# Kernel optimization log

Hardware: AMD Instinct MI355X
Metric: run time of the kernel (lower is better)

The kernel has to match this reference:

```python
import jax, jax.numpy as jnp
import numpy as np

B, N, DIM = 4, 4096, 512
H, DH = 8, 64
F = 256          # nb_features = min(256, int(log(4096)*32)) = 256
CS = 128         # chunk_size = min(128, n)


def setup_inputs() -> dict:
    key = jax.random.key(0)
    k1, k2, k3, k4 = jax.random.split(key, 4)
    x = jax.random.normal(k1, (B, N, DIM), jnp.float32)
    # scale linear weights like default init so activations stay well-conditioned
    w_qkv = jax.random.normal(k2, (3 * H * DH, DIM), jnp.float32) / jnp.sqrt(DIM)
    w_out = jax.random.normal(k3, (DIM, H * DH), jnp.float32) / jnp.sqrt(H * DH)
    b_out = jnp.zeros((DIM,), jnp.float32)
    # torch.qr(randn(F, DH)) -> reduced Q of shape (F, DH), orthonormal columns
    proj = jnp.linalg.qr(jax.random.normal(k4, (F, DH), jnp.float32))[0]
    return {"x": x, "w_qkv": w_qkv, "w_out": w_out, "b_out": b_out, "proj": proj}


def _kernel_fn(t, proj):
    # exp(x @ proj^T - rowmax), stabilized over the feature axis (as in source)
    tp = jnp.einsum('...d,fd->...f', t, proj)
    return jnp.exp(tp - jnp.max(tp, axis=-1, keepdims=True))


def reference(x, w_qkv, w_out, b_out, proj):
    b, n, _ = x.shape
    scale = DH ** -0.5
    c = n // CS  # number of independent local chunks

    qkv = x @ w_qkv.T                                   # [b, n, 3*h*d]
    q, k, v = jnp.split(qkv, 3, axis=-1)

    def to_chunks(t):  # [b, n, h*d] -> [b, h, c, cs, d]
        return t.reshape(b, n, H, DH).transpose(0, 2, 1, 3).reshape(b, H, c, CS, DH)

    q = to_chunks(q) * scale
    k = to_chunks(k)
    v = to_chunks(v)

    q_prime = _kernel_fn(q, proj)                       # [b, h, c, cs, f]
    k_prime = _kernel_fn(k, proj)                       # [b, h, c, cs, f]

    k_sum = k_prime.sum(axis=3)                         # [b, h, c, f]
    D = jnp.einsum('bhcsf,bhcf->bhcs', q_prime, k_sum)
    D_inv = 1.0 / (D + 0.0001)

    context = jnp.einsum('bhcsf,bhcsd->bhcfd', k_prime, v)     # [b, h, c, f, d]
    out = jnp.einsum('bhcsf,bhcfd->bhcsd', q_prime, context)   # [b, h, c, cs, d]
    out = out * D_inv[..., None]

    out = out.reshape(b, H, n, DH).transpose(0, 2, 1, 3).reshape(b, n, H * DH)
    return out @ w_out.T + b_out                        # dropout p=0 -> identity
```

## Files before the change

### kernel.cpp

```cpp
#include <hip/hip_runtime.h>

#define B_ 4
#define N_ 4096
#define DIM_ 512
#define H_ 8
#define DH_ 64
#define F_ 256
#define CS_ 128
#define M_ (B_*N_)
#define NCHUNK_ 1024

typedef __attribute__((ext_vector_type(8))) short bf16x8;
typedef __attribute__((ext_vector_type(4))) float f32x4;

__device__ __forceinline__ unsigned short f2bf(float x){
  unsigned int u = __float_as_uint(x);
  u += 0x7fffu + ((u >> 16) & 1u);
  return (unsigned short)(u >> 16);
}
__device__ __forceinline__ float bf2f(unsigned short s){
  return __uint_as_float(((unsigned int)s) << 16);
}
__device__ __forceinline__ unsigned pack2(float a, float b){
  return (unsigned)f2bf(a) | ((unsigned)f2bf(b) << 16);
}
__device__ __forceinline__ void gl2lds16(const unsigned short* g, unsigned short* l) {
  __builtin_amdgcn_global_load_lds((const __attribute__((address_space(1))) unsigned int*)g,
                                   (__attribute__((address_space(3))) unsigned int*)l,
                                   16, 0, 0);
}

__global__ __launch_bounds__(256)
void split_kernel(const float* __restrict__ src, unsigned short* __restrict__ hi,
                  unsigned short* __restrict__ lo, int n4)
{
  int idx = blockIdx.x * 256 + threadIdx.x;
  if (idx >= n4) return;
  float4 v = ((const float4*)src)[idx];
  unsigned short h0 = f2bf(v.x), h1 = f2bf(v.y), h2 = f2bf(v.z), h3 = f2bf(v.w);
  unsigned short e0 = f2bf(v.x - bf2f(h0)), e1 = f2bf(v.y - bf2f(h1));
  unsigned short e2 = f2bf(v.z - bf2f(h2)), e3 = f2bf(v.w - bf2f(h3));
  uint2 hv, lv;
  hv.x = (unsigned)h0 | ((unsigned)h1 << 16); hv.y = (unsigned)h2 | ((unsigned)h3 << 16);
  lv.x = (unsigned)e0 | ((unsigned)e1 << 16); lv.y = (unsigned)e2 | ((unsigned)e3 << 16);
  ((uint2*)hi)[idx] = hv;
  ((uint2*)lo)[idx] = lv;
}

__global__ __launch_bounds__(256)
void prep_proj(const float* __restrict__ proj, unsigned short* __restrict__ pq,
               unsigned short* __restrict__ pk)
{
  int idx = blockIdx.x * 256 + threadIdx.x;
  if (idx >= 4096) return;
  float4 v = ((const float4*)proj)[idx];
  uint2 k, q;
  k.x = pack2(v.x, v.y);           k.y = pack2(v.z, v.w);
  q.x = pack2(v.x*0.125f, v.y*0.125f); q.y = pack2(v.z*0.125f, v.w*0.125f);
  ((uint2*)pk)[idx] = k;
  ((uint2*)pq)[idx] = q;
}

template<int SPLIT, int OUT>
__global__ __launch_bounds__(256, 2)
void mfma_gemm_nt(const unsigned short* __restrict__ Ahi, const unsigned short* __restrict__ Alo,
                  const unsigned short* __restrict__ Bhi, const unsigned short* __restrict__ Blo,
                  void* __restrict__ Cm, const float* __restrict__ bias, int K, int ldc,
                  unsigned short* __restrict__ vth, unsigned short* __restrict__ vtl)
{
  __shared__ __align__(16) unsigned short sAhi[4096];
  __shared__ __align__(16) unsigned short sBhi[4096];
  __shared__ __align__(16) unsigned short sAlo[4096];
  __shared__ __align__(16) unsigned short sBlo[4096];
  const int tid = threadIdx.x, lane = tid & 63, wave = tid >> 6;
  const int bm = blockIdx.y * 128, bn = blockIdx.x * 128;
  const int srow0 = wave * 32 + (lane >> 2);
  const int srow1 = srow0 + 16;
  const int slot = lane & 3;
  const int g0 = slot ^ ((srow0 >> 1) & 3);
  const int g1 = slot ^ ((srow1 >> 1) & 3);
  const size_t aOff0 = (size_t)(bm + srow0) * K + g0 * 8;
  const size_t aOff1 = (size_t)(bm + srow1) * K + g1 * 8;
  const size_t bOff0 = (size_t)(bn + srow0) * K + g0 * 8;
  const size_t bOff1 = (size_t)(bn + srow1) * K + g1 * 8;
  const int l0 = wave * 1024, l1 = wave * 1024 + 512;
  const int fr = lane & 15, quad = lane >> 4;
  const int wr = (wave >> 1) * 64, wc = (wave & 1) * 64;
  int offA[4], offB[4];
#pragma unroll
  for (int i = 0; i < 4; ++i) {
    int ra = wr + i * 16 + fr;  offA[i] = ra * 32 + (quad ^ ((ra >> 1) & 3)) * 8;
    int rb = wc + i * 16 + fr;  offB[i] = rb * 32 + (quad ^ ((rb >> 1) & 3)) * 8;
  }
  f32x4 acc[4][4];
#pragma unroll
  for (int i = 0; i < 4; ++i)
#pragma unroll
    for (int j = 0; j < 4; ++j) acc[i][j] = {0.f, 0.f, 0.f, 0.f};

  for (int k0 = 0; k0 < K; k0 += 32) {
    gl2lds16(Ahi + aOff0 + k0, &sAhi[l0]);
    gl2lds16(Ahi + aOff1 + k0, &sAhi[l1]);
    gl2lds16(Bhi + bOff0 + k0, &sBhi[l0]);
    gl2lds16(Bhi + bOff1 + k0, &sBhi[l1]);
    if (SPLIT) {
      gl2lds16(Alo + aOff0 + k0, &sAlo[l0]);
      gl2lds16(Alo + aOff1 + k0, &sAlo[l1]);
      gl2lds16(Blo + bOff0 + k0, &sBlo[l0]);
      gl2lds16(Blo + bOff1 + k0, &sBlo[l1]);
    }
    __syncthreads();
    bf16x8 ah[4], bh[4], al[4], bl[4];
#pragma unroll
    for (int i = 0; i < 4; ++i) {
      ah[i] = *(const bf16x8*)&sAhi[offA[i]];
      bh[i] = *(const bf16x8*)&sBhi[offB[i]];
      if (SPLIT) {
        al[i] = *(const bf16x8*)&sAlo[offA[i]];
        bl[i] = *(const bf16x8*)&sBlo[offB[i]];
      }
    }
#pragma unroll
    for (int i = 0; i < 4; ++i)
#pragma unroll
      for (int j = 0; j < 4; ++j) {
        acc[i][j] = __builtin_amdgcn_mfma_f32_16x16x32_bf16(ah[i], bh[j], acc[i][j], 0, 0, 0);
        if (SPLIT) {
          acc[i][j] = __builtin_amdgcn_mfma_f32_16x16x32_bf16(ah[i], bl[j], acc[i][j], 0, 0, 0);
          acc[i][j] = __builtin_amdgcn_mfma_f32_16x16x32_bf16(al[i], bh[j], acc[i][j], 0, 0, 0);
        }
      }
    __syncthreads();
  }
#pragma unroll
  for (int j = 0; j < 4; ++j) {
    int col = bn + wc + j * 16 + fr;
    float bv = (OUT == 0 && bias) ? bias[col] : 0.f;
#pragma unroll
    for (int i = 0; i < 4; ++i) {
      int row0 = bm + wr + i * 16 + quad * 4;
      if (OUT == 0) {
        float* cp = (float*)Cm + (size_t)row0 * ldc + col;
#pragma unroll
        for (int r = 0; r < 4; ++r) cp[(size_t)r * ldc] = acc[i][j][r] + bv;
      } else if (OUT == 1) {
        unsigned short* cp = (unsigned short*)Cm + (size_t)row0 * ldc + col;
#pragma unroll
        for (int r = 0; r < 4; ++r) cp[(size_t)r * ldc] = f2bf(acc[i][j][r]);
      } else {
        int hh = col >> 6, d = col & 63;
        int bb = row0 >> 12, cc2 = (row0 >> 7) & 31, s = row0 & 127;
        int ck = bb * 256 + hh * 32 + cc2;
        size_t ad = (size_t)ck * 8192 + d * 128 + (((s >> 3) ^ (d & 15)) << 3) + (s & 7);
        float v0 = acc[i][j][0], v1 = acc[i][j][1], v2 = acc[i][j][2], v3 = acc[i][j][3];
        unsigned short h0 = f2bf(v0), h1 = f2bf(v1), h2 = f2bf(v2), h3 = f2bf(v3);
        uint2 hv, lv;
        hv.x = (unsigned)h0 | ((unsigned)h1 << 16);
        hv.y = (unsigned)h2 | ((unsigned)h3 << 16);
        lv.x = pack2(v0 - bf2f(h0), v1 - bf2f(h1));
        lv.y = pack2(v2 - bf2f(h2), v3 - bf2f(h3));
        *(uint2*)(vth + ad) = hv;
        *(uint2*)(vtl + ad) = lv;
      }
    }
  }
}

__global__ __launch_bounds__(256, 1)
void fused_chunk(const unsigned short* __restrict__ qkv_bf,
                 const unsigned short* __restrict__ projq,
                 const unsigned short* __restrict__ projk,
                 const unsigned short* __restrict__ vth_g,
                 const unsigned short* __restrict__ vtl_g,
                 unsigned short* __restrict__ attn_hi,
                 unsigned short* __restrict__ attn_lo)
{
  __shared__ __align__(16) char smem[153088];
  unsigned short* KPT = (unsigned short*)smem;
  unsigned short* QP  = (unsigned short*)(smem + 65536);
  unsigned short* X   = (unsigned short*)(smem + 131072);
  float* KS  = (float*)(smem + 147456);
  float* DI  = (float*)(smem + 148480);
  float* KSP = (float*)(smem + 148992);

  const int tid = threadIdx.x, lane = tid & 63, wave = tid >> 6;
  const int fr = lane & 15, quad = lane >> 4;
  const int chunk = blockIdx.x;
  const int b = chunk >> 8, h = (chunk >> 5) & 7, cc = chunk & 31;
  const int mbase = b * N_ + cc * CS_;

#pragma unroll
  for (int j = 0; j < 8; ++j) {
    int idx = tid + j * 256;
    int s = idx >> 4, d0 = (idx & 15) * 4;
    uint2 v = *(const uint2*)(qkv_bf + (size_t)(mbase + s) * 1024 + 512 + h * DH_ + d0);
    *(uint2*)(X + s * 64 + (((d0 >> 3) ^ (s & 7)) << 3) + (d0 & 7)) = v;
  }
  __syncthreads();

  {
    f32x4 ka[2][16];
#pragma unroll
    for (int nt = 0; nt < 16; ++nt) { ka[0][nt] = {0,0,0,0}; ka[1][nt] = {0,0,0,0}; }
#pragma unroll
    for (int ks = 0; ks < 2; ++ks) {
      bf16x8 a[2];
#pragma unroll
      for (int mt = 0; mt < 2; ++mt) {
        int s = wave * 32 + mt * 16 + fr;
        a[mt] = *(const bf16x8*)(X + s * 64 + (((ks * 4 + quad) ^ (s & 7)) << 3));
      }
#pragma unroll
      for (int nt = 0; nt < 16; ++nt) {
        bf16x8 bf = *(const bf16x8*)(projk + (size_t)(nt * 16 + fr) * 64 + ks * 32 + quad * 8);
        ka[0][nt] = __builtin_amdgcn_mfma_f32_16x16x32_bf16(a[0], bf, ka[0][nt], 0, 0, 0);
        ka[1][nt] = __builtin_amdgcn_mfma_f32_16x16x32_bf16(a[1], bf, ka[1][nt], 0, 0, 0);
      }
    }
#pragma unroll
    for (int mt = 0; mt < 2; ++mt)
#pragma unroll
      for (int r = 0; r < 4; ++r) {
        float m = ka[mt][0][r];
#pragma unroll
        for (int nt = 1; nt < 16; ++nt) m = fmaxf(m, ka[mt][nt][r]);
        m = fmaxf(m, __shfl_xor(m, 1, 16));
        m = fmaxf(m, __shfl_xor(m, 2, 16));
        m = fmaxf(m, __shfl_xor(m, 4, 16));
        m = fmaxf(m, __shfl_xor(m, 8, 16));
#pragma unroll
        for (int nt = 0; nt < 16; ++nt) ka[mt][nt][r] = __expf(ka[mt][nt][r] - m);
      }
#pragma unroll
    for (int nt = 0; nt < 16; ++nt) {
      float sm = 0.f;
#pragma unroll
      for (int mt = 0; mt < 2; ++mt)
#pragma unroll
        for (int r = 0; r < 4; ++r) sm += ka[mt][nt][r];
      sm += __shfl_xor(sm, 16, 64);
      sm += __shfl_xor(sm, 32, 64);
      if (quad == 0) KSP[wave * 256 + nt * 16 + fr] = sm;
    }
#pragma unroll
    for (int nt = 0; nt < 16; ++nt) {
      int f = nt * 16 + fr;
#pragma unroll
      for (int mt = 0; mt < 2; ++mt) {
        int g = wave * 4 + mt * 2 + (quad >> 1);
        uint2 w;
        w.x = pack2(ka[mt][nt][0], ka[mt][nt][1]);
        w.y = pack2(ka[mt][nt][2], ka[mt][nt][3]);
        *(uint2*)(KPT + f * 128 + ((g ^ (f & 15)) << 3) + (quad & 1) * 4) = w;
      }
    }
  }
  __syncthreads();

  KS[tid] = KSP[tid] + KSP[256 + tid] + KSP[512 + tid] + KSP[768 + tid];
#pragma unroll
  for (int j = 0; j < 8; ++j) {
    int idx = tid + j * 256;
    int s = idx >> 4, d0 = (idx & 15) * 4;
    uint2 v = *(const uint2*)(qkv_bf + (size_t)(mbase + s) * 1024 + h * DH_ + d0);
    *(uint2*)(X + s * 64 + (((d0 >> 3) ^ (s & 7)) << 3) + (d0 & 7)) = v;
  }
  __syncthreads();

  {
    f32x4 qa[16][2];
#pragma unroll
    for (int mt = 0; mt < 16; ++mt) { qa[mt][0] = {0,0,0,0}; qa[mt][1] = {0,0,0,0}; }
#pragma unroll
    for (int ks = 0; ks < 2; ++ks) {
      bf16x8 bfr[2];
#pragma unroll
      for (int nt = 0; nt < 2; ++nt) {
        int s = wave * 32 + nt * 16 + fr;
        bfr[nt] = *(const bf16x8*)(X + s * 64 + (((ks * 4 + quad) ^ (s & 7)) << 3));
      }
#pragma unroll
      for (int mt = 0; mt < 16; ++mt) {
        bf16x8 af = *(const bf16x8*)(projq + (size_t)(mt * 16 + fr) * 64 + ks * 32 + quad * 8);
        qa[mt][0] = __builtin_amdgcn_mfma_f32_16x16x32_bf16(af, bfr[0], qa[mt][0], 0, 0, 0);
        qa[mt][1] = __builtin_amdgcn_mfma_f32_16x16x32_bf16(af, bfr[1], qa[mt][1], 0, 0, 0);
      }
    }
#pragma unroll
    for (int nt = 0; nt < 2; ++nt) {
      float m = -1e30f;
#pragma unroll
      for (int mt = 0; mt < 16; ++mt)
#pragma unroll
        for (int r = 0; r < 4; ++r) m = fmaxf(m, qa[mt][nt][r]);
      m = fmaxf(m, __shfl_xor(m, 16, 64));
      m = fmaxf(m, __shfl_xor(m, 32, 64));
#pragma unroll
      for (int mt = 0; mt < 16; ++mt)
#pragma unroll
        for (int r = 0; r < 4; ++r) qa[mt][nt][r] = __expf(qa[mt][nt][r] - m);
    }
#pragma unroll
    for (int nt = 0; nt < 2; ++nt) {
      int s = wave * 32 + nt * 16 + fr;
#pragma unroll
      for (int mt = 0; mt < 16; ++mt) {
        int g = mt * 2 + (quad >> 1);
        uint2 w;
        w.x = pack2(qa[mt][nt][0], qa[mt][nt][1]);
        w.y = pack2(qa[mt][nt][2], qa[mt][nt][3]);
        *(uint2*)(QP + s * 256 + ((g ^ (s & 15)) << 3) + (quad & 1) * 4) = w;
      }
    }
  }
  __syncthreads();

  const unsigned short* vhs = vth_g + (size_t)chunk * 8192;
  const unsigned short* vls = vtl_g + (size_t)chunk * 8192;
#pragma unroll
  for (int i = 0; i < 4; ++i) gl2lds16(vhs + (wave*4+i)*512 + lane*8, X + (wave*4+i)*512);
  __syncthreads();

  f32x4 acc_a[4][4];
#pragma unroll
  for (int i = 0; i < 4; ++i)
#pragma unroll
    for (int j = 0; j < 4; ++j) acc_a[i][j] = {0.f, 0.f, 0.f, 0.f};
#pragma unroll
  for (int ks = 0; ks < 4; ++ks) {
    int l = ks * 4 + quad;
    bf16x8 a[4];
#pragma unroll
    for (int mt = 0; mt < 4; ++mt) {
      int f = wave * 64 + mt * 16 + fr;
      a[mt] = *(const bf16x8*)(KPT + f * 128 + ((l ^ (f & 15)) << 3));
    }
#pragma unroll
    for (int nt = 0; nt < 4; ++nt) {
      int d = nt * 16 + fr;
      bf16x8 bh = *(const bf16x8*)(X + d * 128 + ((l ^ (d & 15)) << 3));
#pragma unroll
      for (int mt = 0; mt < 4; ++mt)
        acc_a[mt][nt] = __builtin_amdgcn_mfma_f32_16x16x32_bf16(a[mt], bh, acc_a[mt][nt], 0, 0, 0);
    }
  }
  __syncthreads();
#pragma unroll
  for (int i = 0; i < 4; ++i) gl2lds16(vls + (wave*4+i)*512 + lane*8, X + (wave*4+i)*512);
  __syncthreads();
#pragma unroll
  for (int ks = 0; ks < 4; ++ks) {
    int l = ks * 4 + quad;
    bf16x8 a[4];
#pragma unroll
    for (int mt = 0; mt < 4; ++mt) {
      int f = wave * 64 + mt * 16 + fr;
      a[mt] = *(const bf16x8*)(KPT + f * 128 + ((l ^ (f & 15)) << 3));
    }
#pragma unroll
    for (int nt = 0; nt < 4; ++nt) {
      int d = nt * 16 + fr;
      bf16x8 bl = *(const bf16x8*)(X + d * 128 + ((l ^ (d & 15)) << 3));
#pragma unroll
      for (int mt = 0; mt < 4; ++mt)
        acc_a[mt][nt] = __builtin_amdgcn_mfma_f32_16x16x32_bf16(a[mt], bl, acc_a[mt][nt], 0, 0, 0);
    }
  }
  __syncthreads();

#pragma unroll
  for (int mt = 0; mt < 4; ++mt)
#pragma unroll
    for (int nt = 0; nt < 4; ++nt) {
      int f0 = wave * 64 + mt * 16 + quad * 4;
      int d = nt * 16 + fr;
      int g = wave * 8 + mt * 2 + (quad >> 1);
      float v0 = acc_a[mt][nt][0], v1 = acc_a[mt][nt][1];
      float v2 = acc_a[mt][nt][2], v3 = acc_a[mt][nt][3];
      unsigned short h0 = f2bf(v0), h1 = f2bf(v1), h2 = f2bf(v2), h3 = f2bf(v3);
      uint2 whi, wlo;
      whi.x = (unsigned)h0 | ((unsigned)h1 << 16);
      whi.y = (unsigned)h2 | ((unsigned)h3 << 16);
      wlo.x = pack2(v0 - bf2f(h0), v1 - bf2f(h1));
      wlo.y = pack2(v2 - bf2f(h2), v3 - bf2f(h3));
      int ad = d * 256 + ((g ^ (d & 15)) << 3) + (quad & 1) * 4;
      *(uint2*)(KPT + ad) = whi;
      *(uint2*)(KPT + 16384 + ad) = wlo;
      (void)f0;
    }
  __syncthreads();

  if (tid < 128) {
    int s = tid;
    float dp = 0.f;
#pragma unroll 4
    for (int l = 0; l < 32; ++l) {
      bf16x8 qv = *(const bf16x8*)(QP + s * 256 + ((l ^ (s & 15)) << 3));
      f32x4 k0 = *(const f32x4*)(KS + l * 8);
      f32x4 k1 = *(const f32x4*)(KS + l * 8 + 4);
      dp += bf2f((unsigned short)qv[0]) * k0[0];
      dp += bf2f((unsigned short)qv[1]) * k0[1];
      dp += bf2f((unsigned short)qv[2]) * k0[2];
      dp += bf2f((unsigned short)qv[3]) * k0[3];
      dp += bf2f((unsigned short)qv[4]) * k1[0];
      dp += bf2f((unsigned short)qv[5]) * k1[1];
      dp += bf2f((unsigned short)qv[6]) * k1[2];
      dp += bf2f((unsigned short)qv[7]) * k1[3];
    }
    DI[s] = 1.f / (dp + 1e-4f);
  }
  __syncthreads();

  f32x4 acc2[4][2];
#pragma unroll
  for (int i = 0; i < 4; ++i) { acc2[i][0] = {0,0,0,0}; acc2[i][1] = {0,0,0,0}; }
#pragma unroll
  for (int ks = 0; ks < 8; ++ks) {
    int l = ks * 4 + quad;
    bf16x8 ah[4], al[4];
#pragma unroll
    for (int mt = 0; mt < 4; ++mt) {
      int d = mt * 16 + fr;
      int ad = d * 256 + ((l ^ (d & 15)) << 3);
      ah[mt] = *(const bf16x8*)(KPT + ad);
      al[mt] = *(const bf16x8*)(KPT + 16384 + ad);
    }
#pragma unroll
    for (int nt = 0; nt < 2; ++nt) {
      int s = wave * 32 + nt * 16 + fr;
      bf16x8 bq = *(const bf16x8*)(QP + s * 256 + ((l ^ (s & 15)) << 3));
#pragma unroll
      for (int mt = 0; mt < 4; ++mt) {
        acc2[mt][nt] = __builtin_amdgcn_mfma_f32_16x16x32_bf16(ah[mt], bq, acc2[mt][nt], 0, 0, 0);
        acc2[mt][nt] = __builtin_amdgcn_mfma_f32_16x16x32_bf16(al[mt], bq, acc2[mt][nt], 0, 0, 0);
      }
    }
  }
#pragma unroll
  for (int nt = 0; nt < 2; ++nt) {
    int s = wave * 32 + nt * 16 + fr;
    float di = DI[s];
    size_t base = (size_t)(mbase + s) * 512 + h * DH_;
#pragma unroll
    for (int mt = 0; mt < 4; ++mt) {
      int d0 = mt * 16 + quad * 4;
      float o0 = acc2[mt][nt][0] * di, o1 = acc2[mt][nt][1] * di;
      float o2 = acc2[mt][nt][2] * di, o3 = acc2[mt][nt][3] * di;
      unsigned short h0 = f2bf(o0), h1 = f2bf(o1), h2 = f2bf(o2), h3 = f2bf(o3);
      uint2 whi, wlo;
      whi.x = (unsigned)h0 | ((unsigned)h1 << 16);
      whi.y = (unsigned)h2 | ((unsigned)h3 << 16);
      wlo.x = pack2(o0 - bf2f(h0), o1 - bf2f(h1));
      wlo.y = pack2(o2 - bf2f(h2), o3 - bf2f(h3));
      *(uint2*)(attn_hi + base + d0) = whi;
      *(uint2*)(attn_lo + base + d0) = wlo;
    }
  }
}

extern "C" void kernel_launch(void* const* d_in, const int* in_sizes, int n_in,
                              void* d_out, int out_size, void* d_ws, size_t ws_size,
                              hipStream_t stream)
{
  const float* x     = (const float*)d_in[0];
  const float* w_qkv = (const float*)d_in[1];
  const float* w_out = (const float*)d_in[2];
  const float* b_out = (const float*)d_in[3];
  const float* proj  = (const float*)d_in[4];
  float* out = (float*)d_out;

  char* ws = (char*)d_ws;
  unsigned short* qkv_bf = (unsigned short*)ws;
  unsigned short* x_hi   = (unsigned short*)(ws + 33554432);
  unsigned short* x_lo   = x_hi + (size_t)M_ * DIM_;
  unsigned short* wqkv_hi = (unsigned short*)(ws + 67108864);
  unsigned short* wqkv_lo = wqkv_hi + (size_t)(3*DIM_) * DIM_;
  unsigned short* attn_hi = (unsigned short*)(ws + 134217728);
  unsigned short* attn_lo = attn_hi + (size_t)M_ * DIM_;
  unsigned short* vth_g  = (unsigned short*)(ws + 201326592);
  unsigned short* vtl_g  = (unsigned short*)(ws + 218103808);

  unsigned short* projq = x_hi;
  unsigned short* projk = projq + 16384;
  unsigned short* wout_hi = projk + 16384;
  unsigned short* wout_lo = wout_hi + (size_t)DIM_ * DIM_;

  split_kernel<<<dim3(M_*DIM_/4/256), 256, 0, stream>>>(x, x_hi, x_lo, M_*DIM_/4);
  split_kernel<<<dim3(3*DIM_*DIM_/4/256), 256, 0, stream>>>(w_qkv, wqkv_hi, wqkv_lo, 3*DIM_*DIM_/4);
  mfma_gemm_nt<0,1><<<dim3(8, M_/128), 256, 0, stream>>>(
      x_hi, x_hi, wqkv_hi, wqkv_hi, qkv_bf, nullptr, DIM_, 1024, nullptr, nullptr);
  mfma_gemm_nt<1,2><<<dim3(4, M_/128), 256, 0, stream>>>(
      x_hi, x_lo, wqkv_hi + (size_t)1024*DIM_, wqkv_lo + (size_t)1024*DIM_,
      nullptr, nullptr, DIM_, 0, vth_g, vtl_g);
  prep_proj<<<dim3(16), 256, 0, stream>>>(proj, projq, projk);
  fused_chunk<<<dim3(NCHUNK_), 256, 0, stream>>>(qkv_bf, projq, projk, vth_g, vtl_g,
                                                 attn_hi, attn_lo);
  split_kernel<<<dim3(DIM_*DIM_/4/256), 256, 0, stream>>>(w_out, wout_hi, wout_lo, DIM_*DIM_/4);
  mfma_gemm_nt<1,0><<<dim3(4, M_/128), 256, 0, stream>>>(
      attn_hi, attn_lo, wout_hi, wout_lo, out, b_out, DIM_, DIM_, nullptr, nullptr);
}
```

Baseline: 281.7 us.

## Fold projection into Q/K weights and split fused chunk kernel into stages

Precomputes combined weights W_q·proj^T and W_k·proj^T per head, so the q/k features come straight from x (K=512) instead of computing a Q/K GEMM followed by a K=64 projection. The single large-LDS fused_chunk kernel becomes four smaller kernels (feat_k, feat_q, stepA, stepB) running at two blocks per CU. These kernels pass intermediates (k', q', ksum, D_inv, context) through global memory. This raises occupancy and removes the bf16 qkv intermediate. In exchange it adds a lot of global traffic and more MFMA work, since the feature GEMMs now have K=512 producing 256 features per head.

```diff
diff --git a/kernel.cpp b/kernel.cpp
--- a/kernel.cpp
+++ b/kernel.cpp
@@ -47,18 +47,64 @@
   ((uint2*)lo)[idx] = lv;
 }
 
-__global__ __launch_bounds__(256)
-void prep_proj(const float* __restrict__ proj, unsigned short* __restrict__ pq,
-               unsigned short* __restrict__ pk)
-{
-  int idx = blockIdx.x * 256 + threadIdx.x;
-  if (idx >= 4096) return;
-  float4 v = ((const float4*)proj)[idx];
-  uint2 k, q;
-  k.x = pack2(v.x, v.y);           k.y = pack2(v.z, v.w);
-  q.x = pack2(v.x*0.125f, v.y*0.125f); q.y = pack2(v.z*0.125f, v.w*0.125f);
-  ((uint2*)pk)[idx] = k;
-  ((uint2*)pq)[idx] = q;
+__global__ __launch_bounds__(256, 2)
+void wcomb_kernel(const float* __restrict__ proj, const float* __restrict__ w_qkv,
+                  unsigned short* __restrict__ wqp, unsigned short* __restrict__ wkp)
+{
+  __shared__ float projL[64 * 64];
+  __shared__ float wL[64 * 256];
+  const int h = blockIdx.x, which = blockIdx.y, z = blockIdx.z;
+  const int fbase = (z >> 1) * 64, jbase = (z & 1) * 256;
+  const int tid = threadIdx.x;
+  const float scale = which ? 1.0f : 0.125f;
+#pragma unroll
+  for (int i = 0; i < 16; ++i) {
+    int e = tid + i * 256;
+    int fl = e >> 6, d = e & 63;
+    projL[d * 64 + fl] = proj[(size_t)(fbase + fl) * 64 + d] * scale;
+  }
+  const float* wsrc = w_qkv + (size_t)(which * 512 + h * 64) * 512 + jbase;
+#pragma unroll
+  for (int i = 0; i < 16; ++i) {
+    int e = tid + i * 256;
+    int d = e >> 6, j4 = e & 63;
+    *(float4*)&wL[d * 256 + j4 * 4] = *(const float4*)(wsrc + (size_t)d * 512 + j4 * 4);
+  }
+  __syncthreads();
+  const int tf = tid & 15, tj = tid >> 4;
+  const int f0 = tf * 4, j0 = tj * 16;
+  float acc[4][16];
+#pragma unroll
+  for (int i = 0; i < 4; ++i)
+#pragma unroll
+    for (int j = 0; j < 16; ++j) acc[i][j] = 0.f;
+  for (int d = 0; d < 64; ++d) {
+    float p0 = projL[d*64 + f0], p1 = projL[d*64 + f0 + 1];
+    float p2 = projL[d*64 + f0 + 2], p3 = projL[d*64 + f0 + 3];
+    float4 w0 = *(const float4*)&wL[d*256 + j0];
+    float4 w1 = *(const float4*)&wL[d*256 + j0 + 4];
+    float4 w2 = *(const float4*)&wL[d*256 + j0 + 8];
+    float4 w3 = *(const float4*)&wL[d*256 + j0 + 12];
+    float wv[16] = {w0.x,w0.y,w0.z,w0.w, w1.x,w1.y,w1.z,w1.w,
+                    w2.x,w2.y,w2.z,w2.w, w3.x,w3.y,w3.z,w3.w};
+    float pv[4] = {p0,p1,p2,p3};
+#pragma unroll
+    for (int i = 0; i < 4; ++i)
+#pragma unroll
+      for (int j = 0; j < 16; ++j) acc[i][j] = fmaf(pv[i], wv[j], acc[i][j]);
+  }
+  unsigned short* dst = (which ? wkp : wqp) + (size_t)h * 256 * 512;
+#pragma unroll
+  for (int i = 0; i < 4; ++i) {
+    int f = fbase + f0 + i;
+#pragma unroll
+    for (int c = 0; c < 4; ++c) {
+      uint2 w;
+      w.x = pack2(acc[i][c*4+0], acc[i][c*4+1]);
+      w.y = pack2(acc[i][c*4+2], acc[i][c*4+3]);
+      *(uint2*)(dst + (size_t)f * 512 + jbase + j0 + c * 4) = w;
+    }
+  }
 }
 
 template<int SPLIT, int OUT>
@@ -143,10 +189,6 @@
         float* cp = (float*)Cm + (size_t)row0 * ldc + col;
 #pragma unroll
         for (int r = 0; r < 4; ++r) cp[(size_t)r * ldc] = acc[i][j][r] + bv;
-      } else if (OUT == 1) {
-        unsigned short* cp = (unsigned short*)Cm + (size_t)row0 * ldc + col;
-#pragma unroll
-        for (int r = 0; r < 4; ++r) cp[(size_t)r * ldc] = f2bf(acc[i][j][r]);
       } else {
         int hh = col >> 6, d = col & 63;
         int bb = row0 >> 12, cc2 = (row0 >> 7) & 31, s = row0 & 127;
@@ -166,159 +208,235 @@
   }
 }
 
-__global__ __launch_bounds__(256, 1)
-void fused_chunk(const unsigned short* __restrict__ qkv_bf,
-                 const unsigned short* __restrict__ projq,
-                 const unsigned short* __restrict__ projk,
-                 const unsigned short* __restrict__ vth_g,
-                 const unsigned short* __restrict__ vtl_g,
-                 unsigned short* __restrict__ attn_hi,
-                 unsigned short* __restrict__ attn_lo)
-{
-  __shared__ __align__(16) char smem[153088];
-  unsigned short* KPT = (unsigned short*)smem;
-  unsigned short* QP  = (unsigned short*)(smem + 65536);
-  unsigned short* X   = (unsigned short*)(smem + 131072);
-  float* KS  = (float*)(smem + 147456);
-  float* DI  = (float*)(smem + 148480);
-  float* KSP = (float*)(smem + 148992);
-
+__global__ __launch_bounds__(256, 2)
+void feat_k(const unsigned short* __restrict__ x_hi, const unsigned short* __restrict__ wkp,
+            unsigned short* __restrict__ kpT_g, float* __restrict__ ksum_g)
+{
+  __shared__ __align__(16) char smem[69632];
+  unsigned short* SA = (unsigned short*)smem;
+  unsigned short* SB = SA + 8192;
+  unsigned short* KP = SA;
+  float* KSP = (float*)(smem + 65536);
   const int tid = threadIdx.x, lane = tid & 63, wave = tid >> 6;
   const int fr = lane & 15, quad = lane >> 4;
   const int chunk = blockIdx.x;
   const int b = chunk >> 8, h = (chunk >> 5) & 7, cc = chunk & 31;
   const int mbase = b * N_ + cc * CS_;
-
-#pragma unroll
-  for (int j = 0; j < 8; ++j) {
-    int idx = tid + j * 256;
-    int s = idx >> 4, d0 = (idx & 15) * 4;
-    uint2 v = *(const uint2*)(qkv_bf + (size_t)(mbase + s) * 1024 + 512 + h * DH_ + d0);
-    *(uint2*)(X + s * 64 + (((d0 >> 3) ^ (s & 7)) << 3) + (d0 & 7)) = v;
-  }
-  __syncthreads();
-
-  {
-    f32x4 ka[2][16];
-#pragma unroll
-    for (int nt = 0; nt < 16; ++nt) { ka[0][nt] = {0,0,0,0}; ka[1][nt] = {0,0,0,0}; }
-#pragma unroll
-    for (int ks = 0; ks < 2; ++ks) {
+  const unsigned short* wk = wkp + (size_t)h * 256 * 512;
+
+  f32x4 ka[2][16];
+#pragma unroll
+  for (int nt = 0; nt < 16; ++nt) { ka[0][nt] = {0,0,0,0}; ka[1][nt] = {0,0,0,0}; }
+
+  for (int kit = 0; kit < 8; ++kit) {
+    int k0 = kit * 64;
+#pragma unroll
+    for (int i = 0; i < 4; ++i) {
+      int u = (wave * 4 + i) * 64 + lane;
+      int s = u >> 3, jg = u & 7;
+      gl2lds16(x_hi + (size_t)(mbase + s) * 512 + k0 + ((jg ^ (s & 7)) << 3),
+               SA + (size_t)(wave * 4 + i) * 512);
+    }
+#pragma unroll
+    for (int i = 0; i < 8; ++i) {
+      int u = (wave * 8 + i) * 64 + lane;
+      int f = u >> 3, jg = u & 7;
+      gl2lds16(wk + (size_t)f * 512 + k0 + ((jg ^ (f & 7)) << 3),
+               SB + (size_t)(wave * 8 + i) * 512);
+    }
+    __syncthreads();
+#pragma unroll
+    for (int kin = 0; kin < 2; ++kin) {
+      int g8 = kin * 4 + quad;
       bf16x8 a[2];
 #pragma unroll
       for (int mt = 0; mt < 2; ++mt) {
         int s = wave * 32 + mt * 16 + fr;
-        a[mt] = *(const bf16x8*)(X + s * 64 + (((ks * 4 + quad) ^ (s & 7)) << 3));
+        a[mt] = *(const bf16x8*)(SA + s * 64 + ((g8 ^ (s & 7)) << 3));
       }
 #pragma unroll
       for (int nt = 0; nt < 16; ++nt) {
-        bf16x8 bf = *(const bf16x8*)(projk + (size_t)(nt * 16 + fr) * 64 + ks * 32 + quad * 8);
-        ka[0][nt] = __builtin_amdgcn_mfma_f32_16x16x32_bf16(a[0], bf, ka[0][nt], 0, 0, 0);
-        ka[1][nt] = __builtin_amdgcn_mfma_f32_16x16x32_bf16(a[1], bf, ka[1][nt], 0, 0, 0);
-      }
-    }
+        int f = nt * 16 + fr;
+        bf16x8 bb = *(const bf16x8*)(SB + f * 64 + ((g8 ^ (f & 7)) << 3));
+        ka[0][nt] = __builtin_amdgcn_mfma_f32_16x16x32_bf16(a[0], bb, ka[0][nt], 0, 0, 0);
+        ka[1][nt] = __builtin_amdgcn_mfma_f32_16x16x32_bf16(a[1], bb, ka[1][nt], 0, 0, 0);
+      }
+    }
+    __syncthreads();
+  }
+#pragma unroll
+  for (int mt = 0; mt < 2; ++mt)
+#pragma unroll
+    for (int r = 0; r < 4; ++r) {
+      float m = ka[mt][0][r];
+#pragma unroll
+      for (int nt = 1; nt < 16; ++nt) m = fmaxf(m, ka[mt][nt][r]);
+      m = fmaxf(m, __shfl_xor(m, 1, 16));
+      m = fmaxf(m, __shfl_xor(m, 2, 16));
+      m = fmaxf(m, __shfl_xor(m, 4, 16));
+      m = fmaxf(m, __shfl_xor(m, 8, 16));
+#pragma unroll
+      for (int nt = 0; nt < 16; ++nt) ka[mt][nt][r] = __expf(ka[mt][nt][r] - m);
+    }
+#pragma unroll
+  for (int nt = 0; nt < 16; ++nt) {
+    float sm = 0.f;
 #pragma unroll
     for (int mt = 0; mt < 2; ++mt)
 #pragma unroll
-      for (int r = 0; r < 4; ++r) {
-        float m = ka[mt][0][r];
-#pragma unroll
-        for (int nt = 1; nt < 16; ++nt) m = fmaxf(m, ka[mt][nt][r]);
-        m = fmaxf(m, __shfl_xor(m, 1, 16));
-        m = fmaxf(m, __shfl_xor(m, 2, 16));
-        m = fmaxf(m, __shfl_xor(m, 4, 16));
-        m = fmaxf(m, __shfl_xor(m, 8, 16));
-#pragma unroll
-        for (int nt = 0; nt < 16; ++nt) ka[mt][nt][r] = __expf(ka[mt][nt][r] - m);
-      }
-#pragma unroll
-    for (int nt = 0; nt < 16; ++nt) {
-      float sm = 0.f;
-#pragma unroll
-      for (int mt = 0; mt < 2; ++mt)
-#pragma unroll
-        for (int r = 0; r < 4; ++r) sm += ka[mt][nt][r];
-      sm += __shfl_xor(sm, 16, 64);
-      sm += __shfl_xor(sm, 32, 64);
-      if (quad == 0) KSP[wave * 256 + nt * 16 + fr] = sm;
-    }
-#pragma unroll
-    for (int nt = 0; nt < 16; ++nt) {
-      int f = nt * 16 + fr;
-#pragma unroll
-      for (int mt = 0; mt < 2; ++mt) {
-        int g = wave * 4 + mt * 2 + (quad >> 1);
-        uint2 w;
-        w.x = pack2(ka[mt][nt][0], ka[mt][nt][1]);
-        w.y = pack2(ka[mt][nt][2], ka[mt][nt][3]);
-        *(uint2*)(KPT + f * 128 + ((g ^ (f & 15)) << 3) + (quad & 1) * 4) = w;
-      }
-    }
-  }
-  __syncthreads();
-
-  KS[tid] = KSP[tid] + KSP[256 + tid] + KSP[512 + tid] + KSP[768 + tid];
-#pragma unroll
-  for (int j = 0; j < 8; ++j) {
-    int idx = tid + j * 256;
-    int s = idx >> 4, d0 = (idx & 15) * 4;
-    uint2 v = *(const uint2*)(qkv_bf + (size_t)(mbase + s) * 1024 + h * DH_ + d0);
-    *(uint2*)(X + s * 64 + (((d0 >> 3) ^ (s & 7)) << 3) + (d0 & 7)) = v;
-  }
-  __syncthreads();
-
-  {
-    f32x4 qa[16][2];
-#pragma unroll
-    for (int mt = 0; mt < 16; ++mt) { qa[mt][0] = {0,0,0,0}; qa[mt][1] = {0,0,0,0}; }
-#pragma unroll
-    for (int ks = 0; ks < 2; ++ks) {
-      bf16x8 bfr[2];
+      for (int r = 0; r < 4; ++r) sm += ka[mt][nt][r];
+    sm += __shfl_xor(sm, 16, 64);
+    sm += __shfl_xor(sm, 32, 64);
+    if (quad == 0) KSP[wave * 256 + nt * 16 + fr] = sm;
+  }
+#pragma unroll
+  for (int nt = 0; nt < 16; ++nt) {
+    int f = nt * 16 + fr;
+#pragma unroll
+    for (int mt = 0; mt < 2; ++mt) {
+      int g = wave * 4 + mt * 2 + (quad >> 1);
+      uint2 w;
+      w.x = pack2(ka[mt][nt][0], ka[mt][nt][1]);
+      w.y = pack2(ka[mt][nt][2], ka[mt][nt][3]);
+      *(uint2*)(KP + f * 128 + ((g ^ (f & 15)) << 3) + (quad & 1) * 4) = w;
+    }
+  }
+  __syncthreads();
+  ksum_g[(size_t)chunk * 256 + tid] =
+      KSP[tid] + KSP[256 + tid] + KSP[512 + tid] + KSP[768 + tid];
+#pragma unroll
+  for (int i = 0; i < 16; ++i) {
+    int idx = i * 256 + tid;
+    *(float4*)(kpT_g + (size_t)chunk * 32768 + idx * 8) = *(const float4*)(KP + idx * 8);
+  }
+}
+
+__global__ __launch_bounds__(256, 2)
+void feat_q(const unsigned short* __restrict__ x_hi, const unsigned short* __restrict__ wqp,
+            const float* __restrict__ ksum_g, float* __restrict__ di_g,
+            unsigned short* __restrict__ qp_g)
+{
+  __shared__ __align__(16) char smem[66560];
+  unsigned short* SA = (unsigned short*)smem;
+  unsigned short* SB = SA + 8192;
+  unsigned short* QP = SA;
+  float* KS = (float*)(smem + 65536);
+  const int tid = threadIdx.x, lane = tid & 63, wave = tid >> 6;
+  const int fr = lane & 15, quad = lane >> 4;
+  const int chunk = blockIdx.x;
+  const int b = chunk >> 8, h = (chunk >> 5) & 7, cc = chunk & 31;
+  const int mbase = b * N_ + cc * CS_;
+  const unsigned short* wq = wqp + (size_t)h * 256 * 512;
+
+  KS[tid] = ksum_g[(size_t)chunk * 256 + tid];
+
+  f32x4 qa[16][2];
+#pragma unroll
+  for (int mt = 0; mt < 16; ++mt) { qa[mt][0] = {0,0,0,0}; qa[mt][1] = {0,0,0,0}; }
+
+  for (int kit = 0; kit < 8; ++kit) {
+    int k0 = kit * 64;
+#pragma unroll
+    for (int i = 0; i < 4; ++i) {
+      int u = (wave * 4 + i) * 64 + lane;
+      int s = u >> 3, jg = u & 7;
+      gl2lds16(x_hi + (size_t)(mbase + s) * 512 + k0 + ((jg ^ (s & 7)) << 3),
+               SA + (size_t)(wave * 4 + i) * 512);
+    }
+#pragma unroll
+    for (int i = 0; i < 8; ++i) {
+      int u = (wave * 8 + i) * 64 + lane;
+      int f = u >> 3, jg = u & 7;
+      gl2lds16(wq + (size_t)f * 512 + k0 + ((jg ^ (f & 7)) << 3),
+               SB + (size_t)(wave * 8 + i) * 512);
+    }
+    __syncthreads();
+#pragma unroll
+    for (int kin = 0; kin < 2; ++kin) {
+      int g8 = kin * 4 + quad;
+      bf16x8 bx[2];
 #pragma unroll
       for (int nt = 0; nt < 2; ++nt) {
         int s = wave * 32 + nt * 16 + fr;
-        bfr[nt] = *(const bf16x8*)(X + s * 64 + (((ks * 4 + quad) ^ (s & 7)) << 3));
+        bx[nt] = *(const bf16x8*)(SA + s * 64 + ((g8 ^ (s & 7)) << 3));
       }
 #pragma unroll
       for (int mt = 0; mt < 16; ++mt) {
-        bf16x8 af = *(const bf16x8*)(projq + (size_t)(mt * 16 + fr) * 64 + ks * 32 + quad * 8);
-        qa[mt][0] = __builtin_amdgcn_mfma_f32_16x16x32_bf16(af, bfr[0], qa[mt][0], 0, 0, 0);
-        qa[mt][1] = __builtin_amdgcn_mfma_f32_16x16x32_bf16(af, bfr[1], qa[mt][1], 0, 0, 0);
-      }
-    }
-#pragma unroll
-    for (int nt = 0; nt < 2; ++nt) {
-      float m = -1e30f;
-#pragma unroll
-      for (int mt = 0; mt < 16; ++mt)
-#pragma unroll
-        for (int r = 0; r < 4; ++r) m = fmaxf(m, qa[mt][nt][r]);
-      m = fmaxf(m, __shfl_xor(m, 16, 64));
-      m = fmaxf(m, __shfl_xor(m, 32, 64));
-#pragma unroll
-      for (int mt = 0; mt < 16; ++mt)
-#pragma unroll
-        for (int r = 0; r < 4; ++r) qa[mt][nt][r] = __expf(qa[mt][nt][r] - m);
-    }
-#pragma unroll
-    for (int nt = 0; nt < 2; ++nt) {
+        int f = mt * 16 + fr;
+        bf16x8 af = *(const bf16x8*)(SB + f * 64 + ((g8 ^ (f & 7)) << 3));
+        qa[mt][0] = __builtin_amdgcn_mfma_f32_16x16x32_bf16(af, bx[0], qa[mt][0], 0, 0, 0);
+        qa[mt][1] = __builtin_amdgcn_mfma_f32_16x16x32_bf16(af, bx[1], qa[mt][1], 0, 0, 0);
+      }
+    }
+    __syncthreads();
+  }
+#pragma unroll
+  for (int nt = 0; nt < 2; ++nt) {
+    float m = -1e30f;
+#pragma unroll
+    for (int mt = 0; mt < 16; ++mt)
+#pragma unroll
+      for (int r = 0; r < 4; ++r) m = fmaxf(m, qa[mt][nt][r]);
+    m = fmaxf(m, __shfl_xor(m, 16, 64));
+    m = fmaxf(m, __shfl_xor(m, 32, 64));
+#pragma unroll
+    for (int mt = 0; mt < 16; ++mt)
+#pragma unroll
+      for (int r = 0; r < 4; ++r) qa[mt][nt][r] = __expf(qa[mt][nt][r] - m);
+    float dp = 0.f;
+#pragma unroll
+    for (int mt = 0; mt < 16; ++mt) {
+      f32x4 k4 = *(const f32x4*)(KS + mt * 16 + quad * 4);
+#pragma unroll
+      for (int r = 0; r < 4; ++r) dp = fmaf(qa[mt][nt][r], k4[r], dp);
+    }
+    dp += __shfl_xor(dp, 16, 64);
+    dp += __shfl_xor(dp, 32, 64);
+    if (quad == 0) {
       int s = wave * 32 + nt * 16 + fr;
-#pragma unroll
-      for (int mt = 0; mt < 16; ++mt) {
-        int g = mt * 2 + (quad >> 1);
-        uint2 w;
-        w.x = pack2(qa[mt][nt][0], qa[mt][nt][1]);
-        w.y = pack2(qa[mt][nt][2], qa[mt][nt][3]);
-        *(uint2*)(QP + s * 256 + ((g ^ (s & 15)) << 3) + (quad & 1) * 4) = w;
-      }
-    }
-  }
-  __syncthreads();
-
+      di_g[(size_t)chunk * 128 + s] = 1.f / (dp + 1e-4f);
+    }
+  }
+#pragma unroll
+  for (int nt = 0; nt < 2; ++nt) {
+    int s = wave * 32 + nt * 16 + fr;
+#pragma unroll
+    for (int mt = 0; mt < 16; ++mt) {
+      int g = mt * 2 + (quad >> 1);
+      uint2 w;
+      w.x = pack2(qa[mt][nt][0], qa[mt][nt][1]);
+      w.y = pack2(qa[mt][nt][2], qa[mt][nt][3]);
+      *(uint2*)(QP + s * 256 + ((g ^ (s & 15)) << 3) + (quad & 1) * 4) = w;
+    }
+  }
+  __syncthreads();
+#pragma unroll
+  for (int i = 0; i < 16; ++i) {
+    int idx = i * 256 + tid;
+    *(float4*)(qp_g + (size_t)chunk * 32768 + idx * 8) = *(const float4*)(QP + idx * 8);
+  }
+}
+
+__global__ __launch_bounds__(256, 2)
+void stepA(const unsigned short* __restrict__ kpT_g,
+           const unsigned short* __restrict__ vth_g,
+           const unsigned short* __restrict__ vtl_g,
+           unsigned short* __restrict__ ctx_g)
+{
+  __shared__ __align__(16) char smem[81920];
+  unsigned short* KPT = (unsigned short*)smem;
+  unsigned short* X   = (unsigned short*)(smem + 65536);
+  const int tid = threadIdx.x, lane = tid & 63, wave = tid >> 6;
+  const int fr = lane & 15, quad = lane >> 4;
+  const int chunk = blockIdx.x;
+  const int lofs = lane * 8;
+  const unsigned short* kps = kpT_g + (size_t)chunk * 32768;
   const unsigned short* vhs = vth_g + (size_t)chunk * 8192;
   const unsigned short* vls = vtl_g + (size_t)chunk * 8192;
 #pragma unroll
-  for (int i = 0; i < 4; ++i) gl2lds16(vhs + (wave*4+i)*512 + lane*8, X + (wave*4+i)*512);
+  for (int i = 0; i < 16; ++i) gl2lds16(kps + (wave*16+i)*512 + lofs, KPT + (wave*16+i)*512);
+#pragma unroll
+  for (int i = 0; i < 4; ++i)  gl2lds16(vhs + (wave*4+i)*512 + lofs, X + (wave*4+i)*512);
   __syncthreads();
 
   f32x4 acc_a[4][4];
@@ -346,7 +464,7 @@
   }
   __syncthreads();
 #pragma unroll
-  for (int i = 0; i < 4; ++i) gl2lds16(vls + (wave*4+i)*512 + lane*8, X + (wave*4+i)*512);
+  for (int i = 0; i < 4; ++i)  gl2lds16(vls + (wave*4+i)*512 + lofs, X + (wave*4+i)*512);
   __syncthreads();
 #pragma unroll
   for (int ks = 0; ks < 4; ++ks) {
@@ -372,7 +490,6 @@
   for (int mt = 0; mt < 4; ++mt)
 #pragma unroll
     for (int nt = 0; nt < 4; ++nt) {
-      int f0 = wave * 64 + mt * 16 + quad * 4;
       int d = nt * 16 + fr;
       int g = wave * 8 + mt * 2 + (quad >> 1);
       float v0 = acc_a[mt][nt][0], v1 = acc_a[mt][nt][1];
@@ -386,29 +503,35 @@
       int ad = d * 256 + ((g ^ (d & 15)) << 3) + (quad & 1) * 4;
       *(uint2*)(KPT + ad) = whi;
       *(uint2*)(KPT + 16384 + ad) = wlo;
-      (void)f0;
-    }
-  __syncthreads();
-
-  if (tid < 128) {
-    int s = tid;
-    float dp = 0.f;
-#pragma unroll 4
-    for (int l = 0; l < 32; ++l) {
-      bf16x8 qv = *(const bf16x8*)(QP + s * 256 + ((l ^ (s & 15)) << 3));
-      f32x4 k0 = *(const f32x4*)(KS + l * 8);
-      f32x4 k1 = *(const f32x4*)(KS + l * 8 + 4);
-      dp += bf2f((unsigned short)qv[0]) * k0[0];
-      dp += bf2f((unsigned short)qv[1]) * k0[1];
-      dp += bf2f((unsigned short)qv[2]) * k0[2];
-      dp += bf2f((unsigned short)qv[3]) * k0[3];
-      dp += bf2f((unsigned short)qv[4]) * k1[0];
-      dp += bf2f((unsigned short)qv[5]) * k1[1];
-      dp += bf2f((unsigned short)qv[6]) * k1[2];
-      dp += bf2f((unsigned short)qv[7]) * k1[3];
-    }
-    DI[s] = 1.f / (dp + 1e-4f);
-  }
+    }
+  __syncthreads();
+#pragma unroll
+  for (int i = 0; i < 16; ++i) {
+    int idx = i * 256 + tid;
+    *(float4*)(ctx_g + (size_t)chunk * 32768 + idx * 8) = *(const float4*)(KPT + idx * 8);
+  }
+}
+
+__global__ __launch_bounds__(256, 2)
+void stepB(const unsigned short* __restrict__ ctx_g,
+           const unsigned short* __restrict__ qp_g,
+           const float* __restrict__ di_g,
+           unsigned short* __restrict__ attn_hi,
+           unsigned short* __restrict__ attn_lo)
+{
+  __shared__ __align__(16) char smem[66048];
+  unsigned short* CTX = (unsigned short*)smem;
+  float* DIL = (float*)(smem + 65536);
+  const int tid = threadIdx.x, lane = tid & 63, wave = tid >> 6;
+  const int fr = lane & 15, quad = lane >> 4;
+  const int chunk = blockIdx.x;
+  const int b = chunk >> 8, h = (chunk >> 5) & 7, cc = chunk & 31;
+  const int mbase = b * N_ + cc * CS_;
+  const unsigned short* cs = ctx_g + (size_t)chunk * 32768;
+  const unsigned short* qps = qp_g + (size_t)chunk * 32768;
+#pragma unroll
+  for (int i = 0; i < 16; ++i) gl2lds16(cs + (wave*16+i)*512 + lane*8, CTX + (wave*16+i)*512);
+  if (tid < 128) DIL[tid] = di_g[(size_t)chunk * 128 + tid];
   __syncthreads();
 
   f32x4 acc2[4][2];
@@ -417,29 +540,29 @@
 #pragma unroll
   for (int ks = 0; ks < 8; ++ks) {
     int l = ks * 4 + quad;
-    bf16x8 ah[4], al[4];
+    bf16x8 bq[2];
+#pragma unroll
+    for (int nt = 0; nt < 2; ++nt) {
+      int s = wave * 32 + nt * 16 + fr;
+      bq[nt] = *(const bf16x8*)(qps + s * 256 + ((l ^ (s & 15)) << 3));
+    }
 #pragma unroll
     for (int mt = 0; mt < 4; ++mt) {
       int d = mt * 16 + fr;
       int ad = d * 256 + ((l ^ (d & 15)) << 3);
-      ah[mt] = *(const bf16x8*)(KPT + ad);
-      al[mt] = *(const bf16x8*)(KPT + 16384 + ad);
-    }
-#pragma unroll
-    for (int nt = 0; nt < 2; ++nt) {
-      int s = wave * 32 + nt * 16 + fr;
-      bf16x8 bq = *(const bf16x8*)(QP + s * 256 + ((l ^ (s & 15)) << 3));
-#pragma unroll
-      for (int mt = 0; mt < 4; ++mt) {
-        acc2[mt][nt] = __builtin_amdgcn_mfma_f32_16x16x32_bf16(ah[mt], bq, acc2[mt][nt], 0, 0, 0);
-        acc2[mt][nt] = __builtin_amdgcn_mfma_f32_16x16x32_bf16(al[mt], bq, acc2[mt][nt], 0, 0, 0);
+      bf16x8 ah = *(const bf16x8*)(CTX + ad);
+      bf16x8 al = *(const bf16x8*)(CTX + 16384 + ad);
+#pragma unroll
+      for (int nt = 0; nt < 2; ++nt) {
+        acc2[mt][nt] = __builtin_amdgcn_mfma_f32_16x16x32_bf16(ah, bq[nt], acc2[mt][nt], 0, 0, 0);
+        acc2[mt][nt] = __builtin_amdgcn_mfma_f32_16x16x32_bf16(al, bq[nt], acc2[mt][nt], 0, 0, 0);
       }
     }
   }
 #pragma unroll
   for (int nt = 0; nt < 2; ++nt) {
     int s = wave * 32 + nt * 16 + fr;
-    float di = DI[s];
+    float di = DIL[s];
     size_t base = (size_t)(mbase + s) * 512 + h * DH_;
 #pragma unroll
     for (int mt = 0; mt < 4; ++mt) {
@@ -470,32 +593,35 @@
   float* out = (float*)d_out;
 
   char* ws = (char*)d_ws;
-  unsigned short* qkv_bf = (unsigned short*)ws;
-  unsigned short* x_hi   = (unsigned short*)(ws + 33554432);
-  unsigned short* x_lo   = x_hi + (size_t)M_ * DIM_;
-  unsigned short* wqkv_hi = (unsigned short*)(ws + 67108864);
-  unsigned short* wqkv_lo = wqkv_hi + (size_t)(3*DIM_) * DIM_;
-  unsigned short* attn_hi = (unsigned short*)(ws + 134217728);
-  unsigned short* attn_lo = attn_hi + (size_t)M_ * DIM_;
-  unsigned short* vth_g  = (unsigned short*)(ws + 201326592);
-  unsigned short* vtl_g  = (unsigned short*)(ws + 218103808);
-
-  unsigned short* projq = x_hi;
-  unsigned short* projk = projq + 16384;
-  unsigned short* wout_hi = projk + 16384;
-  unsigned short* wout_lo = wout_hi + (size_t)DIM_ * DIM_;
+  unsigned short* x_hi   = (unsigned short*)ws;
+  unsigned short* x_lo   = (unsigned short*)(ws + 16777216);
+  unsigned short* wv_hi  = (unsigned short*)(ws + 33554432);
+  unsigned short* wv_lo  = (unsigned short*)(ws + 34078720);
+  unsigned short* wout_hi= (unsigned short*)(ws + 34603008);
+  unsigned short* wout_lo= (unsigned short*)(ws + 35127296);
+  unsigned short* wqp    = (unsigned short*)(ws + 35651584);
+  unsigned short* wkp    = (unsigned short*)(ws + 37748736);
+  unsigned short* vth_g  = (unsigned short*)(ws + 39845888);
+  unsigned short* vtl_g  = (unsigned short*)(ws + 56623104);
+  unsigned short* kpT_g  = (unsigned short*)(ws + 73400320);
+  unsigned short* ctx_g  = kpT_g;
+  unsigned short* qp_g   = (unsigned short*)(ws + 140509184);
+  float*          ksum_g = (float*)(ws + 207618048);
+  float*          di_g   = (float*)(ws + 208666624);
+  unsigned short* attn_hi = x_hi;
+  unsigned short* attn_lo = x_lo;
 
   split_kernel<<<dim3(M_*DIM_/4/256), 256, 0, stream>>>(x, x_hi, x_lo, M_*DIM_/4);
-  split_kernel<<<dim3(3*DIM_*DIM_/4/256), 256, 0, stream>>>(w_qkv, wqkv_hi, wqkv_lo, 3*DIM_*DIM_/4);
-  mfma_gemm_nt<0,1><<<dim3(8, M_/128), 256, 0, stream>>>(
-      x_hi, x_hi, wqkv_hi, wqkv_hi, qkv_bf, nullptr, DIM_, 1024, nullptr, nullptr);
+  split_kernel<<<dim3(DIM_*DIM_/4/256), 256, 0, stream>>>(w_qkv + (size_t)1024*DIM_,
+                                                          wv_hi, wv_lo, DIM_*DIM_/4);
+  split_kernel<<<dim3(DIM_*DIM_/4/256), 256, 0, stream>>>(w_out, wout_hi, wout_lo, DIM_*DIM_/4);
+  wcomb_kernel<<<dim3(8, 2, 8), 256, 0, stream>>>(proj, w_qkv, wqp, wkp);
   mfma_gemm_nt<1,2><<<dim3(4, M_/128), 256, 0, stream>>>(
-      x_hi, x_lo, wqkv_hi + (size_t)1024*DIM_, wqkv_lo + (size_t)1024*DIM_,
-      nullptr, nullptr, DIM_, 0, vth_g, vtl_g);
-  prep_proj<<<dim3(16), 256, 0, stream>>>(proj, projq, projk);
-  fused_chunk<<<dim3(NCHUNK_), 256, 0, stream>>>(qkv_bf, projq, projk, vth_g, vtl_g,
-                                                 attn_hi, attn_lo);
-  split_kernel<<<dim3(DIM_*DIM_/4/256), 256, 0, stream>>>(w_out, wout_hi, wout_lo, DIM_*DIM_/4);
+      x_hi, x_lo, wv_hi, wv_lo, nullptr, nullptr, DIM_, 0, vth_g, vtl_g);
+  feat_k<<<dim3(NCHUNK_), 256, 0, stream>>>(x_hi, wkp, kpT_g, ksum_g);
+  feat_q<<<dim3(NCHUNK_), 256, 0, stream>>>(x_hi, wqp, ksum_g, di_g, qp_g);
+  stepA<<<dim3(NCHUNK_), 256, 0, stream>>>(kpT_g, vth_g, vtl_g, ctx_g);
+  stepB<<<dim3(NCHUNK_), 256, 0, stream>>>(ctx_g, qp_g, di_g, attn_hi, attn_lo);
   mfma_gemm_nt<1,0><<<dim3(4, M_/128), 256, 0, stream>>>(
       attn_hi, attn_lo, wout_hi, wout_lo, out, b_out, DIM_, DIM_, nullptr, nullptr);
 }
```

New measurement: 324.8 us. 15.3% more time.
